# Performance work log

Hardware: AMD Instinct MI355X
Metric: run time of the kernel (lower is better)

## Reference

```python
import jax, jax.numpy as jnp
import numpy as np
from jax import lax

B, T, I, H, O = 256, 2048, 50, 116, 50


def setup_inputs() -> dict:
    key = jax.random.key(0)
    ks = jax.random.split(key, 7)
    k = 1.0 / np.sqrt(H)  # torch default uniform init bound for nn.RNN / nn.Linear
    u = lambda kk, shp: jax.random.uniform(kk, shp, jnp.float32, -k, k)
    return {
        "x": jax.random.normal(ks[0], (B, T, I), jnp.float32),
        "W_ih": u(ks[1], (H, I)),
        "b_ih": u(ks[2], (H,)),
        "W_hh": u(ks[3], (H, H)),
        "b_hh": u(ks[4], (H,)),
        "W_fc": u(ks[5], (O, H)),
        "b_fc": u(ks[6], (O,)),
    }


def reference(x, W_ih, b_ih, W_hh, b_hh, W_fc, b_fc):
    # Precompute input contribution for all timesteps: [B, T, H]
    xp = jnp.einsum("bti,hi->bth", x, W_ih) + b_ih + b_hh

    def step(h, xt):
        # h: [B, H], xt: [B, H]; Elman ReLU cell
        h_new = jax.nn.relu(xt + h @ W_hh.T)
        return h_new, h_new

    h0 = jnp.zeros((x.shape[0], W_hh.shape[0]), x.dtype)
    _, hs = lax.scan(step, h0, jnp.swapaxes(xp, 0, 1))  # hs: [T, B, H]
    out = jnp.swapaxes(hs, 0, 1)  # [B, T, H]
    out = jax.nn.relu(out)  # trailing ReLU (no-op after ReLU cell, kept for fidelity)
    return out @ W_fc.T + b_fc  # [B, T, O]
```

## Files before the change

kernel.cpp:

```cpp
#include <hip/hip_runtime.h>


namespace {
constexpr int kB = 256;
constexpr int kT = 2048;
constexpr int kI = 50;
constexpr int kH = 116;
constexpr int kO = 50;
constexpr int kSS = 8;
constexpr int kHD = 16;
constexpr int kXPD = 16;
}

struct Smem {
  alignas(16) float h[kHD][144];
  alignas(16) float xp[kXPD][128];
  alignas(16) float xr[4][52];
  int flags[2];
};

__device__ __forceinline__ void sync_lds() {
  __asm__ __volatile__("s_waitcnt lgkmcnt(0)\n\ts_barrier" ::: "memory");
}

__device__ __forceinline__ void wait_flag(const volatile int* f, int want) {
  while (__builtin_amdgcn_readfirstlane(*f) < want) {}
  __asm__ __volatile__("" ::: "memory");
}

__device__ __forceinline__ float qadd1(float v) {
  return v + __int_as_float(__builtin_amdgcn_update_dpp(
                 0, __float_as_int(v), 0xB1, 0xF, 0xF, true));
}
__device__ __forceinline__ float qadd2(float v) {
  return v + __int_as_float(__builtin_amdgcn_update_dpp(
                 0, __float_as_int(v), 0x4E, 0xF, 0xF, true));
}

__device__ __forceinline__ void h_step(Smem& sm, int t, const float (&w)[4][32],
                                       int k, int rowk, int hwr, bool wvalid) {
  const float xpv = sm.xp[t & (kXPD - 1)][rowk];
  const float4* hp4 = (const float4*)sm.h[(t + kHD - 1) & (kHD - 1)];
  float4 hc[8];
#pragma unroll
  for (int i = 0; i < 8; ++i) hc[i] = hp4[9 * k + i];
  float res = 0.f;
#pragma unroll
  for (int p = 0; p < 4; ++p) {
    float s0 = 0.f, s1 = 0.f, s2 = 0.f, s3 = 0.f;
#pragma unroll
    for (int i = 0; i < 8; ++i) {
      const float4 v = hc[i];
      s0 = fmaf(w[p][4 * i + 0], v.x, s0);
      s1 = fmaf(w[p][4 * i + 1], v.y, s1);
      s2 = fmaf(w[p][4 * i + 2], v.z, s2);
      s3 = fmaf(w[p][4 * i + 3], v.w, s3);
    }
    float c = (s0 + s1) + (s2 + s3);
    c = qadd2(qadd1(c));
    res = (k == p) ? c : res;
  }
  res += xpv;
  res = res > 0.f ? res : 0.f;
  if (wvalid) sm.h[t & (kHD - 1)][hwr] = res;
}

__device__ __forceinline__ void fc_step(Smem& sm, int u, const float (&w)[4][32],
                                        int k, int rowk, float bfc,
                                        float* __restrict__ ob) {
  const float4* hp4 = (const float4*)sm.h[u & (kHD - 1)];
  float4 hc[8];
#pragma unroll
  for (int i = 0; i < 8; ++i) hc[i] = hp4[9 * k + i];
  float res = 0.f;
#pragma unroll
  for (int p = 0; p < 4; ++p) {
    float s0 = 0.f, s1 = 0.f, s2 = 0.f, s3 = 0.f;
#pragma unroll
    for (int i = 0; i < 8; ++i) {
      const float4 v = hc[i];
      s0 = fmaf(w[p][4 * i + 0], v.x, s0);
      s1 = fmaf(w[p][4 * i + 1], v.y, s1);
      s2 = fmaf(w[p][4 * i + 2], v.z, s2);
      s3 = fmaf(w[p][4 * i + 3], v.w, s3);
    }
    float c = (s0 + s1) + (s2 + s3);
    c = qadd2(qadd1(c));
    res = (k == p) ? c : res;
  }
  res += bfc;
  if (rowk < kO) ob[(size_t)u * kO + rowk] = res;
}

__device__ __forceinline__ void xp_step(Smem& sm, int xs, int slot,
                                        const float (&wi0)[kI],
                                        const float (&wi1)[kI],
                                        float bias0, float bias1, int ln) {
  const float4* xq = (const float4*)sm.xr[xs];
  float s00 = 0.f, s01 = 0.f, s02 = 0.f, s03 = 0.f;
  float s10 = 0.f, s11 = 0.f, s12 = 0.f, s13 = 0.f;
#pragma unroll
  for (int i = 0; i < 12; ++i) {
    float4 v = xq[i];
    s00 = fmaf(wi0[4 * i + 0], v.x, s00);
    s01 = fmaf(wi0[4 * i + 1], v.y, s01);
    s02 = fmaf(wi0[4 * i + 2], v.z, s02);
    s03 = fmaf(wi0[4 * i + 3], v.w, s03);
    s10 = fmaf(wi1[4 * i + 0], v.x, s10);
    s11 = fmaf(wi1[4 * i + 1], v.y, s11);
    s12 = fmaf(wi1[4 * i + 2], v.z, s12);
    s13 = fmaf(wi1[4 * i + 3], v.w, s13);
  }
  float2 vt = ((const float2*)sm.xr[xs])[24];
  s00 = fmaf(wi0[48], vt.x, s00);
  s01 = fmaf(wi0[49], vt.y, s01);
  s10 = fmaf(wi1[48], vt.x, s10);
  s11 = fmaf(wi1[49], vt.y, s11);
  sm.xp[slot][ln] = bias0 + ((s00 + s01) + (s02 + s03));
  if (ln < kH - 64) sm.xp[slot][ln + 64] = bias1 + ((s10 + s11) + (s12 + s13));
}

__launch_bounds__(256, 1)
__global__ void rnn_fused(const float* __restrict__ x,
                          const float* __restrict__ W_ih,
                          const float* __restrict__ b_ih,
                          const float* __restrict__ W_hh,
                          const float* __restrict__ b_hh,
                          const float* __restrict__ W_fc,
                          const float* __restrict__ b_fc,
                          float* __restrict__ out) {
  __shared__ Smem sm;
  const int tid = threadIdx.x;
  const int wv = tid >> 6;
  const int ln = tid & 63;
  const int b = blockIdx.x;
  const float* xb = x + (size_t)b * (kT * kI);
  float* ob = out + (size_t)b * (kT * kO);

  float w[4][32];
  float wi0[kI], wi1[kI];
  float bias0 = 0.f, bias1 = 0.f, bfc = 0.f;
  float xrv[4] = {0.f, 0.f, 0.f, 0.f};

  const int k = ln & 3;
  const int rl = ln >> 2;
  int rowk = 0, hwr = 0;
  bool wvalid = false;

  if (wv < 2) {
    const int rbase = 58 * wv;
    rowk = rbase + rl + 16 * k;
    wvalid = (rl + 16 * k) < 58;
    hwr = 36 * (rowk >> 5) + (rowk & 31);
#pragma unroll
    for (int p = 0; p < 4; ++p) {
      const int rloc = rl + 16 * p;
      const bool vr = rloc < 58;
      const size_t r = rbase + (vr ? rloc : 0);
#pragma unroll
      for (int j = 0; j < 32; ++j) {
        const int col = 32 * k + j;
        w[p][j] = (vr && col < kH) ? W_hh[r * kH + col] : 0.f;
      }
    }
  } else if (wv == 2) {
    rowk = rl + 16 * k;
#pragma unroll
    for (int p = 0; p < 4; ++p) {
      const int rloc = rl + 16 * p;
      const bool vr = rloc < kO;
      const size_t r = vr ? rloc : 0;
#pragma unroll
      for (int j = 0; j < 32; ++j) {
        const int col = 32 * k + j;
        w[p][j] = (vr && col < kH) ? W_fc[r * kH + col] : 0.f;
      }
    }
    bfc = (rowk < kO) ? b_fc[rowk] : 0.f;
  } else {
    {
      const float2* wr = (const float2*)(W_ih + ln * kI);
#pragma unroll
      for (int i = 0; i < kI / 2; ++i) {
        float2 v = wr[i]; wi0[2 * i] = v.x; wi0[2 * i + 1] = v.y;
      }
      bias0 = b_ih[ln] + b_hh[ln];
    }
    if (ln < kH - 64) {
      const float2* wr = (const float2*)(W_ih + (ln + 64) * kI);
#pragma unroll
      for (int i = 0; i < kI / 2; ++i) {
        float2 v = wr[i]; wi1[2 * i] = v.x; wi1[2 * i + 1] = v.y;
      }
      bias1 = b_ih[ln + 64] + b_hh[ln + 64];
    } else {
#pragma unroll
      for (int i = 0; i < kI; ++i) wi1[i] = 0.f;
    }
    if (ln < kI) {
      sm.xr[0][ln] = xb[0 * kI + ln];
      sm.xr[1][ln] = xb[1 * kI + ln];
      xrv[2] = xb[2 * kI + ln];
      xrv[3] = xb[3 * kI + ln];
      xrv[0] = xb[4 * kI + ln];
      xrv[1] = xb[5 * kI + ln];
    }
  }
  if (tid < 144) sm.h[kHD - 1][tid] = 0.f;
  if (tid == 0) { sm.flags[0] = -1; sm.flags[1] = -1; }
  sync_lds();

  if (wv < 2) __builtin_amdgcn_s_setprio(1);

  if (wv == 3) {
#pragma unroll
    for (int j = 0; j < kSS; ++j) {
      xp_step(sm, j & 3, j & (kXPD - 1), wi0, wi1, bias0, bias1, ln);
      if (ln < kI) {
        sm.xr[(j + 2) & 3][ln] = xrv[(j + 2) & 3];
        const int tf = j + 6;
        xrv[(j + 2) & 3] = xb[(size_t)tf * kI + ln];
      }
    }
  }
  sync_lds();

  volatile int* my = (volatile int*)&sm.flags[wv & 1];
  const volatile int* oth = (const volatile int*)&sm.flags[1 - (wv & 1)];

#pragma unroll 1
  for (int s = 0; s < kT / kSS; ++s) {
    if (wv < 2) {
      const int t0 = kSS * s;
#pragma unroll
      for (int j = 0; j < kSS; ++j) {
        const int t = t0 + j;
        if (j > 0) wait_flag(oth, t - 1);
        h_step(sm, t, w, k, rowk, hwr, wvalid);
        __asm__ __volatile__("" ::: "memory");
        if (ln == 0) *my = t;
      }
    } else if (wv == 2) {
      if (s > 0) {
        const int u0 = kSS * (s - 1);
#pragma unroll
        for (int j = 0; j < kSS; ++j)
          fc_step(sm, u0 + j, w, k, rowk, bfc, ob);
      }
    } else {
      if (s < kT / kSS - 1) {
        const int tau0 = kSS * s + kSS;
#pragma unroll
        for (int j = 0; j < kSS; ++j) {
          const int tau = tau0 + j;
          xp_step(sm, j & 3, tau & (kXPD - 1), wi0, wi1, bias0, bias1, ln);
          if (ln < kI) {
            sm.xr[(j + 2) & 3][ln] = xrv[(j + 2) & 3];
            int tf = tau + 6; tf = tf < kT ? tf : kT - 1;
            xrv[(j + 2) & 3] = xb[(size_t)tf * kI + ln];
          }
        }
      }
    }
    sync_lds();
  }

  if (wv == 2) {
#pragma unroll
    for (int j = 0; j < kSS; ++j)
      fc_step(sm, kT - kSS + j, w, k, rowk, bfc, ob);
  }
}

extern "C" void kernel_launch(void* const* d_in, const int* in_sizes, int n_in,
                              void* d_out, int out_size, void* d_ws, size_t ws_size,
                              hipStream_t stream) {
  (void)in_sizes; (void)n_in; (void)d_ws; (void)ws_size; (void)out_size;
  const float* x    = (const float*)d_in[0];
  const float* W_ih = (const float*)d_in[1];
  const float* b_ih = (const float*)d_in[2];
  const float* W_hh = (const float*)d_in[3];
  const float* b_hh = (const float*)d_in[4];
  const float* W_fc = (const float*)d_in[5];
  const float* b_fc = (const float*)d_in[6];
  float* out = (float*)d_out;
  rnn_fused<<<dim3(kB), dim3(256), 0, stream>>>(x, W_ih, b_ih, W_hh, b_hh,
                                                W_fc, b_fc, out);
}
```

Baseline: 1.056 ms.

## Split recurrent matvec so each wave computes own half before waiting on peer

The hidden-state layout is permuted so each of the two recurrent waves writes its 58 rows into its own half of every lane group's LDS slice. Each wave first accumulates the partial dot product over its own previously written half, then polls the peer's flag and only then reads the peer's half. This hides part of the inter-wave handshake latency behind useful FMAs. It also remaps the W_hh/W_fc column loading to match the new layout, zeroes the whole h ring buffer, and raises the recurrent waves' priority. The risk is more accumulator registers and an extra flag read per step.

```diff
diff --git a/kernel.cpp b/kernel.cpp
--- a/kernel.cpp
+++ b/kernel.cpp
@@ -37,32 +37,69 @@
                  0, __float_as_int(v), 0x4E, 0xF, 0xF, true));
 }
 
-__device__ __forceinline__ void h_step(Smem& sm, int t, const float (&w)[4][32],
-                                       int k, int rowk, int hwr, bool wvalid) {
+template <int OWN_OFF>
+__device__ __forceinline__ void h_step2(Smem& sm, int t, const float (&w)[4][32],
+                                        int k, int rowk, int hwr, bool wvalid,
+                                        bool need_poll, const volatile int* oth,
+                                        volatile int* my, int ln) {
+  int fl = 0;
+  if (need_poll) fl = __builtin_amdgcn_readfirstlane(*oth);
   const float xpv = sm.xp[t & (kXPD - 1)][rowk];
   const float4* hp4 = (const float4*)sm.h[(t + kHD - 1) & (kHD - 1)];
-  float4 hc[8];
-#pragma unroll
-  for (int i = 0; i < 8; ++i) hc[i] = hp4[9 * k + i];
+  float s[4][4];
+#pragma unroll
+  for (int p = 0; p < 4; ++p) {
+    s[p][0] = 0.f; s[p][1] = 0.f; s[p][2] = 0.f; s[p][3] = 0.f;
+  }
+  {
+    float4 hc[4];
+#pragma unroll
+    for (int i = 0; i < 4; ++i) hc[i] = hp4[9 * k + OWN_OFF + i];
+#pragma unroll
+    for (int p = 0; p < 4; ++p) {
+#pragma unroll
+      for (int i = 0; i < 4; ++i) {
+        const float4 v = hc[i];
+        constexpr int B = 4 * OWN_OFF;
+        s[p][0] = fmaf(w[p][B + 4 * i + 0], v.x, s[p][0]);
+        s[p][1] = fmaf(w[p][B + 4 * i + 1], v.y, s[p][1]);
+        s[p][2] = fmaf(w[p][B + 4 * i + 2], v.z, s[p][2]);
+        s[p][3] = fmaf(w[p][B + 4 * i + 3], v.w, s[p][3]);
+      }
+    }
+  }
+  if (need_poll && fl < t - 1) wait_flag(oth, t - 1);
+  __asm__ __volatile__("" ::: "memory");
+  {
+    constexpr int OO = 4 - OWN_OFF;
+    float4 hc[4];
+#pragma unroll
+    for (int i = 0; i < 4; ++i) hc[i] = hp4[9 * k + OO + i];
+#pragma unroll
+    for (int p = 0; p < 4; ++p) {
+#pragma unroll
+      for (int i = 0; i < 4; ++i) {
+        const float4 v = hc[i];
+        constexpr int B = 4 * OO;
+        s[p][0] = fmaf(w[p][B + 4 * i + 0], v.x, s[p][0]);
+        s[p][1] = fmaf(w[p][B + 4 * i + 1], v.y, s[p][1]);
+        s[p][2] = fmaf(w[p][B + 4 * i + 2], v.z, s[p][2]);
+        s[p][3] = fmaf(w[p][B + 4 * i + 3], v.w, s[p][3]);
+      }
+    }
+  }
   float res = 0.f;
 #pragma unroll
   for (int p = 0; p < 4; ++p) {
-    float s0 = 0.f, s1 = 0.f, s2 = 0.f, s3 = 0.f;
-#pragma unroll
-    for (int i = 0; i < 8; ++i) {
-      const float4 v = hc[i];
-      s0 = fmaf(w[p][4 * i + 0], v.x, s0);
-      s1 = fmaf(w[p][4 * i + 1], v.y, s1);
-      s2 = fmaf(w[p][4 * i + 2], v.z, s2);
-      s3 = fmaf(w[p][4 * i + 3], v.w, s3);
-    }
-    float c = (s0 + s1) + (s2 + s3);
+    float c = (s[p][0] + s[p][1]) + (s[p][2] + s[p][3]);
     c = qadd2(qadd1(c));
     res = (k == p) ? c : res;
   }
   res += xpv;
   res = res > 0.f ? res : 0.f;
   if (wvalid) sm.h[t & (kHD - 1)][hwr] = res;
+  __asm__ __volatile__("" ::: "memory");
+  if (ln == 0) *my = t;
 }
 
 __device__ __forceinline__ void fc_step(Smem& sm, int u, const float (&w)[4][32],
@@ -151,7 +188,7 @@
     const int rbase = 58 * wv;
     rowk = rbase + rl + 16 * k;
     wvalid = (rl + 16 * k) < 58;
-    hwr = 36 * (rowk >> 5) + (rowk & 31);
+    hwr = 36 * k + (wv == 0 ? rl : 16 + rl);
 #pragma unroll
     for (int p = 0; p < 4; ++p) {
       const int rloc = rl + 16 * p;
@@ -159,8 +196,10 @@
       const size_t r = rbase + (vr ? rloc : 0);
 #pragma unroll
       for (int j = 0; j < 32; ++j) {
-        const int col = 32 * k + j;
-        w[p][j] = (vr && col < kH) ? W_hh[r * kH + col] : 0.f;
+        const int cc = 16 * k + (j < 16 ? j : j - 16);
+        const bool cv = cc < 58;
+        const int ca = (j < 16) ? cc : 58 + cc;
+        w[p][j] = (vr && cv) ? W_hh[r * kH + ca] : 0.f;
       }
     }
   } else if (wv == 2) {
@@ -172,8 +211,10 @@
       const size_t r = vr ? rloc : 0;
 #pragma unroll
       for (int j = 0; j < 32; ++j) {
-        const int col = 32 * k + j;
-        w[p][j] = (vr && col < kH) ? W_fc[r * kH + col] : 0.f;
+        const int cc = 16 * k + (j < 16 ? j : j - 16);
+        const bool cv = cc < 58;
+        const int ca = (j < 16) ? cc : 58 + cc;
+        w[p][j] = (vr && cv) ? W_fc[r * kH + ca] : 0.f;
       }
     }
     bfc = (rowk < kO) ? b_fc[rowk] : 0.f;
@@ -206,11 +247,11 @@
       xrv[1] = xb[5 * kI + ln];
     }
   }
-  if (tid < 144) sm.h[kHD - 1][tid] = 0.f;
+  for (int z = tid; z < kHD * 144; z += 256) ((float*)sm.h)[z] = 0.f;
   if (tid == 0) { sm.flags[0] = -1; sm.flags[1] = -1; }
   sync_lds();
 
-  if (wv < 2) __builtin_amdgcn_s_setprio(1);
+  if (wv < 2) __builtin_amdgcn_s_setprio(2);
 
   if (wv == 3) {
 #pragma unroll
@@ -230,16 +271,16 @@
 
 #pragma unroll 1
   for (int s = 0; s < kT / kSS; ++s) {
-    if (wv < 2) {
+    if (wv == 0) {
       const int t0 = kSS * s;
 #pragma unroll
-      for (int j = 0; j < kSS; ++j) {
-        const int t = t0 + j;
-        if (j > 0) wait_flag(oth, t - 1);
-        h_step(sm, t, w, k, rowk, hwr, wvalid);
-        __asm__ __volatile__("" ::: "memory");
-        if (ln == 0) *my = t;
-      }
+      for (int j = 0; j < kSS; ++j)
+        h_step2<0>(sm, t0 + j, w, k, rowk, hwr, wvalid, j > 0, oth, my, ln);
+    } else if (wv == 1) {
+      const int t0 = kSS * s;
+#pragma unroll
+      for (int j = 0; j < kSS; ++j)
+        h_step2<4>(sm, t0 + j, w, k, rowk, hwr, wvalid, j > 0, oth, my, ln);
     } else if (wv == 2) {
       if (s > 0) {
         const int u0 = kSS * (s - 1);
```

Result: slower. 1.251 ms (+18.5%).

## Speculate h loads before flag poll and use readlane for x projection

Applied to the files above, without the earlier changes.

The recurrent step now reads the flag and issues the LDS loads of the previous hidden state speculatively, re-polling and reloading only if the partner wave has not yet published. This takes the flag-wait round trip off the serial critical path. The input-projection wave now keeps x values in registers and broadcasts them with readlane instead of staging them through an LDS buffer, which removes LDS writes and barriers-dependent traffic. The whole h buffer is zero-initialised so speculative reads of stale slots stay benign; the speculation relies on the memory ordering of the volatile flag read relative to the LDS loads.

```diff
diff --git a/kernel.cpp b/kernel.cpp
--- a/kernel.cpp
+++ b/kernel.cpp
@@ -15,17 +15,11 @@
 struct Smem {
   alignas(16) float h[kHD][144];
   alignas(16) float xp[kXPD][128];
-  alignas(16) float xr[4][52];
   int flags[2];
 };
 
 __device__ __forceinline__ void sync_lds() {
   __asm__ __volatile__("s_waitcnt lgkmcnt(0)\n\ts_barrier" ::: "memory");
-}
-
-__device__ __forceinline__ void wait_flag(const volatile int* f, int want) {
-  while (__builtin_amdgcn_readfirstlane(*f) < want) {}
-  __asm__ __volatile__("" ::: "memory");
 }
 
 __device__ __forceinline__ float qadd1(float v) {
@@ -38,12 +32,26 @@
 }
 
 __device__ __forceinline__ void h_step(Smem& sm, int t, const float (&w)[4][32],
-                                       int k, int rowk, int hwr, bool wvalid) {
+                                       int k, int rowk, int hwr, bool wvalid,
+                                       bool need_poll,
+                                       const volatile int* oth,
+                                       volatile int* my, int ln) {
+  const float4* hp4 = (const float4*)sm.h[(t + kHD - 1) & (kHD - 1)];
+  int fl = 0;
+  if (need_poll) {
+    fl = *oth;
+    __asm__ __volatile__("" ::: "memory");
+  }
   const float xpv = sm.xp[t & (kXPD - 1)][rowk];
-  const float4* hp4 = (const float4*)sm.h[(t + kHD - 1) & (kHD - 1)];
   float4 hc[8];
 #pragma unroll
   for (int i = 0; i < 8; ++i) hc[i] = hp4[9 * k + i];
+  if (need_poll && __builtin_amdgcn_readfirstlane(fl) < t - 1) {
+    while (__builtin_amdgcn_readfirstlane(*oth) < t - 1) {}
+    __asm__ __volatile__("" ::: "memory");
+#pragma unroll
+    for (int i = 0; i < 8; ++i) hc[i] = hp4[9 * k + i];
+  }
   float res = 0.f;
 #pragma unroll
   for (int p = 0; p < 4; ++p) {
@@ -63,6 +71,8 @@
   res += xpv;
   res = res > 0.f ? res : 0.f;
   if (wvalid) sm.h[t & (kHD - 1)][hwr] = res;
+  __asm__ __volatile__("" ::: "memory");
+  if (ln == 0) *my = t;
 }
 
 __device__ __forceinline__ void fc_step(Smem& sm, int u, const float (&w)[4][32],
@@ -92,30 +102,34 @@
   if (rowk < kO) ob[(size_t)u * kO + rowk] = res;
 }
 
-__device__ __forceinline__ void xp_step(Smem& sm, int xs, int slot,
-                                        const float (&wi0)[kI],
-                                        const float (&wi1)[kI],
-                                        float bias0, float bias1, int ln) {
-  const float4* xq = (const float4*)sm.xr[xs];
+__device__ __forceinline__ void xp_step_rl(Smem& sm, int slot, float xv,
+                                           const float (&wi0)[kI],
+                                           const float (&wi1)[kI],
+                                           float bias0, float bias1, int ln) {
+  const int xvi = __float_as_int(xv);
   float s00 = 0.f, s01 = 0.f, s02 = 0.f, s03 = 0.f;
   float s10 = 0.f, s11 = 0.f, s12 = 0.f, s13 = 0.f;
 #pragma unroll
   for (int i = 0; i < 12; ++i) {
-    float4 v = xq[i];
-    s00 = fmaf(wi0[4 * i + 0], v.x, s00);
-    s01 = fmaf(wi0[4 * i + 1], v.y, s01);
-    s02 = fmaf(wi0[4 * i + 2], v.z, s02);
-    s03 = fmaf(wi0[4 * i + 3], v.w, s03);
-    s10 = fmaf(wi1[4 * i + 0], v.x, s10);
-    s11 = fmaf(wi1[4 * i + 1], v.y, s11);
-    s12 = fmaf(wi1[4 * i + 2], v.z, s12);
-    s13 = fmaf(wi1[4 * i + 3], v.w, s13);
-  }
-  float2 vt = ((const float2*)sm.xr[xs])[24];
-  s00 = fmaf(wi0[48], vt.x, s00);
-  s01 = fmaf(wi0[49], vt.y, s01);
-  s10 = fmaf(wi1[48], vt.x, s10);
-  s11 = fmaf(wi1[49], vt.y, s11);
+    const float x0 = __int_as_float(__builtin_amdgcn_readlane(xvi, 4 * i + 0));
+    const float x1 = __int_as_float(__builtin_amdgcn_readlane(xvi, 4 * i + 1));
+    const float x2 = __int_as_float(__builtin_amdgcn_readlane(xvi, 4 * i + 2));
+    const float x3 = __int_as_float(__builtin_amdgcn_readlane(xvi, 4 * i + 3));
+    s00 = fmaf(wi0[4 * i + 0], x0, s00);
+    s01 = fmaf(wi0[4 * i + 1], x1, s01);
+    s02 = fmaf(wi0[4 * i + 2], x2, s02);
+    s03 = fmaf(wi0[4 * i + 3], x3, s03);
+    s10 = fmaf(wi1[4 * i + 0], x0, s10);
+    s11 = fmaf(wi1[4 * i + 1], x1, s11);
+    s12 = fmaf(wi1[4 * i + 2], x2, s12);
+    s13 = fmaf(wi1[4 * i + 3], x3, s13);
+  }
+  const float x48 = __int_as_float(__builtin_amdgcn_readlane(xvi, 48));
+  const float x49 = __int_as_float(__builtin_amdgcn_readlane(xvi, 49));
+  s00 = fmaf(wi0[48], x48, s00);
+  s01 = fmaf(wi0[49], x49, s01);
+  s10 = fmaf(wi1[48], x48, s10);
+  s11 = fmaf(wi1[49], x49, s11);
   sm.xp[slot][ln] = bias0 + ((s00 + s01) + (s02 + s03));
   if (ln < kH - 64) sm.xp[slot][ln + 64] = bias1 + ((s10 + s11) + (s12 + s13));
 }
@@ -198,15 +212,11 @@
       for (int i = 0; i < kI; ++i) wi1[i] = 0.f;
     }
     if (ln < kI) {
-      sm.xr[0][ln] = xb[0 * kI + ln];
-      sm.xr[1][ln] = xb[1 * kI + ln];
-      xrv[2] = xb[2 * kI + ln];
-      xrv[3] = xb[3 * kI + ln];
-      xrv[0] = xb[4 * kI + ln];
-      xrv[1] = xb[5 * kI + ln];
-    }
-  }
-  if (tid < 144) sm.h[kHD - 1][tid] = 0.f;
+#pragma unroll
+      for (int q = 0; q < 4; ++q) xrv[q] = xb[(size_t)q * kI + ln];
+    }
+  }
+  for (int z = tid; z < kHD * 144; z += 256) ((float*)sm.h)[z] = 0.f;
   if (tid == 0) { sm.flags[0] = -1; sm.flags[1] = -1; }
   sync_lds();
 
@@ -215,12 +225,8 @@
   if (wv == 3) {
 #pragma unroll
     for (int j = 0; j < kSS; ++j) {
-      xp_step(sm, j & 3, j & (kXPD - 1), wi0, wi1, bias0, bias1, ln);
-      if (ln < kI) {
-        sm.xr[(j + 2) & 3][ln] = xrv[(j + 2) & 3];
-        const int tf = j + 6;
-        xrv[(j + 2) & 3] = xb[(size_t)tf * kI + ln];
-      }
+      xp_step_rl(sm, j & (kXPD - 1), xrv[j & 3], wi0, wi1, bias0, bias1, ln);
+      if (ln < kI) xrv[j & 3] = xb[(size_t)(j + 4) * kI + ln];
     }
   }
   sync_lds();
@@ -233,13 +239,8 @@
     if (wv < 2) {
       const int t0 = kSS * s;
 #pragma unroll
-      for (int j = 0; j < kSS; ++j) {
-        const int t = t0 + j;
-        if (j > 0) wait_flag(oth, t - 1);
-        h_step(sm, t, w, k, rowk, hwr, wvalid);
-        __asm__ __volatile__("" ::: "memory");
-        if (ln == 0) *my = t;
-      }
+      for (int j = 0; j < kSS; ++j)
+        h_step(sm, t0 + j, w, k, rowk, hwr, wvalid, j > 0, oth, my, ln);
     } else if (wv == 2) {
       if (s > 0) {
         const int u0 = kSS * (s - 1);
@@ -253,11 +254,11 @@
 #pragma unroll
         for (int j = 0; j < kSS; ++j) {
           const int tau = tau0 + j;
-          xp_step(sm, j & 3, tau & (kXPD - 1), wi0, wi1, bias0, bias1, ln);
+          xp_step_rl(sm, tau & (kXPD - 1), xrv[j & 3], wi0, wi1, bias0, bias1,
+                     ln);
           if (ln < kI) {
-            sm.xr[(j + 2) & 3][ln] = xrv[(j + 2) & 3];
-            int tf = tau + 6; tf = tf < kT ? tf : kT - 1;
-            xrv[(j + 2) & 3] = xb[(size_t)tf * kI + ln];
+            int tf = tau + 4; tf = tf < kT ? tf : kT - 1;
+            xrv[j & 3] = xb[(size_t)tf * kI + ln];
           }
         }
       }
```

Measured after the change: 1.076 ms. No clear change (+1.9%).
